# Performance work log

Measured on AMD Instinct MI355X. Metric: run time of the kernel, lower is better.

## Reference

```python
import jax, jax.numpy as jnp
import numpy as np


def _lstm_cell(x, h, c, w_ih, w_hh, b_ih, b_hh):
    # PyTorch LSTMCell gate order: i, f, g, o
    z = x @ w_ih.T + h @ w_hh.T + b_ih + b_hh
    i, f, g, o = jnp.split(z, 4, axis=-1)
    c_new = jax.nn.sigmoid(f) * c + jax.nn.sigmoid(i) * jnp.tanh(g)
    h_new = jax.nn.sigmoid(o) * jnp.tanh(c_new)
    return h_new, c_new


def setup_inputs() -> dict:
    B, T_in, T_out = 32, 512, 512
    n_mel, n_frames = 80, 1
    n_enc, n_att, n_filt, K = 512, 128, 32, 31
    n_arnn, n_drnn, n_pre = 1024, 1024, 256
    keys = jax.random.split(jax.random.key(0), 25)
    r = lambda k, *s: jax.random.normal(keys[k], s, dtype=jnp.float32) * 0.05
    return {
        "memory": jax.random.normal(keys[0], (B, T_in, n_enc), dtype=jnp.float32),
        "decoder_inputs": jax.random.normal(keys[1], (B, n_mel, T_out), dtype=jnp.float32),
        "memory_lengths": jax.random.randint(keys[2], (B,), T_in // 2, T_in + 1).astype(jnp.int32),
        "prenet_w1": r(3, n_pre, n_mel * n_frames),
        "prenet_w2": r(4, n_pre, n_pre),
        "arnn_w_ih": r(5, 4 * n_arnn, n_pre + n_enc),
        "arnn_w_hh": r(6, 4 * n_arnn, n_arnn),
        "arnn_b_ih": r(7, 4 * n_arnn),
        "arnn_b_hh": r(8, 4 * n_arnn),
        "query_w": r(9, n_att, n_arnn),
        "memory_w": r(10, n_att, n_enc),
        "v_w": r(11, 1, n_att),
        "loc_conv_w": r(12, n_filt, 2, K),
        "loc_dense_w": r(13, n_att, n_filt),
        "drnn_w_ih": r(14, 4 * n_drnn, n_arnn + n_enc),
        "drnn_w_hh": r(15, 4 * n_drnn, n_drnn),
        "drnn_b_ih": r(16, 4 * n_drnn),
        "drnn_b_hh": r(17, 4 * n_drnn),
        "proj_w": r(18, n_mel * n_frames, n_drnn + n_enc),
        "proj_b": r(19, n_mel * n_frames),
        "gate_w": r(20, 1, n_drnn + n_enc),
        "gate_b": r(21, 1),
    }


def reference(memory, decoder_inputs, memory_lengths, prenet_w1, prenet_w2,
              arnn_w_ih, arnn_w_hh, arnn_b_ih, arnn_b_hh,
              query_w, memory_w, v_w, loc_conv_w, loc_dense_w,
              drnn_w_ih, drnn_w_hh, drnn_b_ih, drnn_b_hh,
              proj_w, proj_b, gate_w, gate_b):
    B, T_in, n_enc = memory.shape
    n_mel, T_out = decoder_inputs.shape[1], decoder_inputs.shape[2]
    n_arnn = arnn_w_hh.shape[1]
    n_drnn = drnn_w_hh.shape[1]
    K = loc_conv_w.shape[-1]
    dt = memory.dtype

    # mask: True = padded position (masked_fill with -inf in torch)
    mask = jnp.arange(T_in)[None, :] >= memory_lengths[:, None]          # (B, T_in)
    processed_memory = memory @ memory_w.T                               # (B, T_in, n_att)

    # teacher-forced inputs with go frame: (T_out+1, B, n_mel)
    go = jnp.zeros((1, B, n_mel), dt)
    dec_in = jnp.concatenate([go, jnp.transpose(decoder_inputs, (2, 0, 1))], 0)
    # prenet (dropout omitted for a deterministic reference)
    pre = jax.nn.relu(dec_in @ prenet_w1.T)
    pre = jax.nn.relu(pre @ prenet_w2.T)[:-1]                            # (T_out, B, n_pre)

    init = (jnp.zeros((B, n_arnn), dt), jnp.zeros((B, n_arnn), dt),
            jnp.zeros((B, n_drnn), dt), jnp.zeros((B, n_drnn), dt),
            jnp.zeros((B, T_in), dt), jnp.zeros((B, T_in), dt),
            jnp.zeros((B, n_enc), dt))

    def step(carry, pre_t):
        ah, ac, dh, dc, aw, aw_cum, actx = carry
        # attention RNN
        ah, ac = _lstm_cell(jnp.concatenate([pre_t, actx], -1), ah, ac,
                            arnn_w_ih, arnn_w_hh, arnn_b_ih, arnn_b_hh)
        # location-sensitive attention
        aw_cat = jnp.stack([aw, aw_cum], axis=1)                         # (B, 2, T_in)
        loc = jax.lax.conv_general_dilated(
            aw_cat, loc_conv_w, (1,), [(K // 2, K // 2)],
            dimension_numbers=("NCH", "OIH", "NCH"))                   # (B, n_filt, T_in)
        loc = jnp.transpose(loc, (0, 2, 1)) @ loc_dense_w.T              # (B, T_in, n_att)
        pq = (ah @ query_w.T)[:, None, :]                                # (B, 1, n_att)
        e = (jnp.tanh(pq + loc + processed_memory) @ v_w.T)[..., 0]      # (B, T_in)
        e = jnp.where(mask, -jnp.inf, e)
        aw = jax.nn.softmax(e, axis=1)
        actx = jnp.einsum("bt,bte->be", aw, memory)                      # (B, n_enc)
        aw_cum = aw_cum + aw
        # decoder RNN
        dh, dc = _lstm_cell(jnp.concatenate([ah, actx], -1), dh, dc,
                            drnn_w_ih, drnn_w_hh, drnn_b_ih, drnn_b_hh)
        dhc = jnp.concatenate([dh, actx], -1)
        mel = dhc @ proj_w.T + proj_b
        gate = (dhc @ gate_w.T + gate_b)[:, 0]
        return (ah, ac, dh, dc, aw, aw_cum, actx), (mel, gate, aw)

    _, (mels, gates, aligns) = jax.lax.scan(step, init, pre)
    mel_outputs = jnp.transpose(mels, (1, 2, 0))        # (B, n_mel, T_out)
    gate_outputs = gates.T                              # (B, T_out)
    alignments = jnp.transpose(aligns, (1, 0, 2))       # (B, T_out, T_in)
    return mel_outputs, gate_outputs, alignments
```

## Files before the change

kernel.cpp:

```cpp
#include <hip/hip_runtime.h>
#include <math.h>

#define NB 32
#define TIN 512
#define TOUT 512
#define NENC 512
#define NATT 128
#define NU 1024
#define NG 4096
#define NPRE 256
#define NMEL 80

#define WS_AH    0u
#define WS_AC    32768u
#define WS_DH    65536u
#define WS_DC    98304u
#define WS_ACTX  131072u
#define WS_AW    147456u
#define WS_AWCUM 163840u
#define WS_E     180224u
#define WS_PQ    196608u
#define WS_ZD    200704u
#define WS_ZA    2822144u
#define WS_PM    4657152u
#define WS_PRE   6754304u
#define WS_WBF   10956800u
#define WS_STATE_ZERO_BYTES (200704u * 4u)
#define OUT_ALIGN ((size_t)NB * NMEL * TOUT + (size_t)NB * TOUT)

#define BW_DIH 0u
#define BW_DHH 6291456u
#define BW_AIH 10485760u
#define BW_AHH 13631488u

__device__ __forceinline__ float fsigm(float x) { return 1.f / (1.f + __expf(-x)); }
__device__ __forceinline__ float ftanh(float x) { return 1.f - 2.f / (__expf(2.f * x) + 1.f); }
__device__ __forceinline__ float bf2f(unsigned short h) { return __uint_as_float((unsigned)h << 16); }

__global__ __launch_bounds__(256) void packbf_kernel(const float* __restrict__ src,
                                                     unsigned short* __restrict__ dst, int n) {
    for (int i = blockIdx.x * 256 + threadIdx.x; i < n; i += gridDim.x * 256) {
        unsigned u = __float_as_uint(src[i]);
        dst[i] = (unsigned short)((u + 0x7FFFu + ((u >> 16) & 1u)) >> 16);
    }
}

__global__ __launch_bounds__(256) void prenet1_kernel(const float* __restrict__ dec,
                                                      const float* __restrict__ w1,
                                                      float* __restrict__ pre) {
    int t = blockIdx.x;
    __shared__ float xl[NB][NMEL];
    for (int i = threadIdx.x; i < NB * NMEL; i += 256) {
        int b = i / NMEL, m = i % NMEL;
        xl[b][m] = (t == 0) ? 0.0f : dec[(b * NMEL + m) * TOUT + (t - 1)];
    }
    __syncthreads();
    int j = threadIdx.x;
    float acc[NB];
#pragma unroll
    for (int b = 0; b < NB; b++) acc[b] = 0.0f;
    for (int m = 0; m < NMEL; m++) {
        float w = w1[j * NMEL + m];
#pragma unroll
        for (int b = 0; b < NB; b++) acc[b] += xl[b][m] * w;
    }
    for (int b = 0; b < NB; b++) pre[((size_t)t * NB + b) * NPRE + j] = fmaxf(acc[b], 0.0f);
}

__global__ __launch_bounds__(256) void prenet2_kernel(const float* __restrict__ w2,
                                                      float* __restrict__ pre) {
    int t = blockIdx.x;
    __shared__ float hl[NB][NPRE];
    for (int i = threadIdx.x; i < NB * NPRE; i += 256)
        hl[i / NPRE][i % NPRE] = pre[(size_t)t * NB * NPRE + i];
    __syncthreads();
    int j = threadIdx.x;
    float acc[NB];
#pragma unroll
    for (int b = 0; b < NB; b++) acc[b] = 0.0f;
    for (int k = 0; k < NPRE; k++) {
        float w = w2[j * NPRE + k];
#pragma unroll
        for (int b = 0; b < NB; b++) acc[b] += hl[b][k] * w;
    }
    for (int b = 0; b < NB; b++) pre[((size_t)t * NB + b) * NPRE + j] = fmaxf(acc[b], 0.0f);
}

__global__ __launch_bounds__(128) void pm_kernel(const float* __restrict__ mem,
                                                 const float* __restrict__ mw,
                                                 float* __restrict__ pm) {
    int b = blockIdx.y, t0 = blockIdx.x * 4;
    __shared__ float ml[4][NENC];
    for (int i = threadIdx.x; i < 4 * NENC; i += 128)
        ml[i / NENC][i % NENC] = mem[((size_t)b * TIN + t0 + i / NENC) * NENC + (i % NENC)];
    __syncthreads();
    int a = threadIdx.x;
    float acc[4] = {0, 0, 0, 0};
    for (int e = 0; e < NENC; e++) {
        float w = mw[a * NENC + e];
#pragma unroll
        for (int tt = 0; tt < 4; tt++) acc[tt] += ml[tt][e] * w;
    }
    for (int tt = 0; tt < 4; tt++)
        pm[((size_t)b * TIN + t0 + tt) * NATT + a] = acc[tt];
}

__global__ __launch_bounds__(256) void z_fused_kernel(
        const unsigned short* __restrict__ wbf,
        const float* __restrict__ ws_base, const float* __restrict__ pre_t,
        float* __restrict__ zd, float* __restrict__ za, int sbase) {
    int col = blockIdx.x * 256 + threadIdx.x;
    int s = blockIdx.y + sbase;
    const float* ah   = ws_base + WS_AH;
    const float* dh   = ws_base + WS_DH;
    const float* actx = ws_base + WS_ACTX;
    const unsigned short* W; const float* x; int xs;
    if (s < 8)       { W = wbf + BW_DIH + (size_t)col * 1536 + s * 128;              x = ah + s * 128;           xs = NU;   }
    else if (s < 12) { W = wbf + BW_DIH + (size_t)col * 1536 + 1024 + (s - 8) * 128; x = actx + (s - 8) * 128;   xs = NENC; }
    else if (s < 20) { W = wbf + BW_DHH + (size_t)col * 1024 + (s - 12) * 128;       x = dh + (s - 12) * 128;    xs = NU;   }
    else if (s < 22) { W = wbf + BW_AIH + (size_t)col * 768 + (s - 20) * 128;        x = pre_t + (s - 20) * 128; xs = NPRE; }
    else if (s < 26) { W = wbf + BW_AIH + (size_t)col * 768 + 256 + (s - 22) * 128;  x = actx + (s - 22) * 128;  xs = NENC; }
    else             { W = wbf + BW_AHH + (size_t)col * 1024 + (s - 26) * 128;       x = ah + (s - 26) * 128;    xs = NU;   }

    float acc[NB];
#pragma unroll
    for (int b = 0; b < NB; b++) acc[b] = 0.0f;
    for (int k4 = 0; k4 < 32; k4++) {
        ushort4 h4 = *(const ushort4*)(W + k4 * 4);
        float w0 = bf2f(h4.x), w1 = bf2f(h4.y), w2 = bf2f(h4.z), w3 = bf2f(h4.w);
#pragma unroll
        for (int b = 0; b < NB; b++) {
            float4 x4 = *(const float4*)(x + (size_t)b * xs + k4 * 4);
            acc[b] = fmaf(w0, x4.x, acc[b]);
            acc[b] = fmaf(w1, x4.y, acc[b]);
            acc[b] = fmaf(w2, x4.z, acc[b]);
            acc[b] = fmaf(w3, x4.w, acc[b]);
        }
    }
    float* zp = ((s < 20) ? (zd + (size_t)s * NB * NG) : (za + (size_t)(s - 20) * NB * NG)) + col;
#pragma unroll
    for (int b = 0; b < NB; b++) zp[(size_t)b * NG] = acc[b];
}

__global__ __launch_bounds__(128) void energies_kernel(const float* __restrict__ pm,
                                                       const float* __restrict__ wc,
                                                       const float* __restrict__ ldw,
                                                       const float* __restrict__ vw,
                                                       const int* __restrict__ mlen,
                                                       const float* __restrict__ ws_aw,
                                                       const float* __restrict__ ws_awcum,
                                                       const float* __restrict__ ws_pq,
                                                       float* __restrict__ ws_e) {
    int b = blockIdx.y, tc = blockIdx.x;
    int tt = threadIdx.x & 31, sub = threadIdx.x >> 5;
    int t = tc * 32 + tt;
    __shared__ float awl[TIN], cuml[TIN], locl[32][33], pql[NATT], ep[32][4];
    for (int i = threadIdx.x; i < TIN; i += 128) {
        awl[i]  = ws_aw[b * TIN + i];
        cuml[i] = ws_awcum[b * TIN + i];
    }
    for (int i = threadIdx.x; i < NATT; i += 128) pql[i] = ws_pq[b * NATT + i];
    __syncthreads();
    for (int f = sub * 8; f < sub * 8 + 8; f++) {
        float s = 0.0f;
        const float* wA = wc + f * 62;
        const float* wB = wA + 31;
        for (int d = 0; d < 31; d++) {
            int tp = t + d - 15;
            if (tp >= 0 && tp < TIN) s += awl[tp] * wA[d] + cuml[tp] * wB[d];
        }
        locl[tt][f] = s;
    }
    __syncthreads();
    float acc = 0.0f;
    const float* pmb = pm + ((size_t)b * TIN + t) * NATT;
    for (int a = sub * 32; a < sub * 32 + 32; a++) {
        float s = pql[a] + pmb[a];
        const float* lw = ldw + a * 32;
#pragma unroll
        for (int f = 0; f < 32; f++) s += locl[tt][f] * lw[f];
        acc += tanhf(s) * vw[a];
    }
    ep[tt][sub] = acc;
    __syncthreads();
    if (sub == 0) {
        float ev = ep[tt][0] + ep[tt][1] + ep[tt][2] + ep[tt][3];
        if (t >= mlen[b]) ev = -3.0e38f;
        ws_e[b * TIN + t] = ev;
    }
}

__global__ __launch_bounds__(256) void softmax_ctx_kernel(const float* __restrict__ mem,
                                                          const float* __restrict__ E,
                                                          float* __restrict__ AW,
                                                          float* __restrict__ AWCUM,
                                                          float* __restrict__ ACTX,
                                                          float* __restrict__ out_align, int step) {
    int b = blockIdx.y, ec = blockIdx.x;
    __shared__ float el[TIN];
    __shared__ float red[256];
    __shared__ float part[4][64];
    const float* Eb = E + b * TIN;
    for (int i = threadIdx.x; i < TIN; i += 256) el[i] = Eb[i];
    __syncthreads();
    red[threadIdx.x] = fmaxf(el[threadIdx.x], el[threadIdx.x + 256]);
    __syncthreads();
    for (int s = 128; s > 0; s >>= 1) {
        if (threadIdx.x < s) red[threadIdx.x] = fmaxf(red[threadIdx.x], red[threadIdx.x + s]);
        __syncthreads();
    }
    float mx = red[0];
    __syncthreads();
    float p0 = __expf(el[threadIdx.x] - mx), p1 = __expf(el[threadIdx.x + 256] - mx);
    el[threadIdx.x] = p0; el[threadIdx.x + 256] = p1;
    red[threadIdx.x] = p0 + p1;
    __syncthreads();
    for (int s = 128; s > 0; s >>= 1) {
        if (threadIdx.x < s) red[threadIdx.x] += red[threadIdx.x + s];
        __syncthreads();
    }
    float inv = 1.0f / red[0];
    int ei = ec * 64 + (threadIdx.x & 63), tp4 = threadIdx.x >> 6;
    float acc = 0.0f;
    const float* mb = mem + (size_t)b * TIN * NENC + ei;
    for (int t = tp4 * 128; t < tp4 * 128 + 128; t++) acc += el[t] * mb[(size_t)t * NENC];
    part[tp4][threadIdx.x & 63] = acc;
    __syncthreads();
    if (threadIdx.x < 64) {
        float ctx = (part[0][threadIdx.x] + part[1][threadIdx.x] +
                     part[2][threadIdx.x] + part[3][threadIdx.x]) * inv;
        ACTX[b * NENC + ec * 64 + threadIdx.x] = ctx;
    }
    if (ec == 0) {
        for (int i = threadIdx.x; i < TIN; i += 256) {
            float a_ = el[i] * inv;
            AW[b * TIN + i] = a_;
            AWCUM[b * TIN + i] += a_;
            out_align[((size_t)b * TOUT + step) * TIN + i] = a_;
        }
    }
}

__global__ __launch_bounds__(512) void gates_kernel(
        const float* __restrict__ abih, const float* __restrict__ abhh,
        const float* __restrict__ qw,
        const float* __restrict__ dbih, const float* __restrict__ dbhh,
        const float* __restrict__ pjw, const float* __restrict__ pjb,
        const float* __restrict__ gtw, const float* __restrict__ gtb,
        float* __restrict__ ws, float* __restrict__ out, int t) {
    __shared__ float sm[NU + NENC];
    int tid = threadIdx.x, bid = blockIdx.x;
    if (bid < 32) {
        if (t < 0) return;
        int b = bid;
        float* DH = ws + WS_DH + (size_t)b * NU;
        float* DC = ws + WS_DC + (size_t)b * NU;
        for (int u = tid; u < NU; u += 512) {
            float zi = dbih[u]          + dbhh[u];
            float zf = dbih[NU + u]     + dbhh[NU + u];
            float zg = dbih[2 * NU + u] + dbhh[2 * NU + u];
            float zo = dbih[3 * NU + u] + dbhh[3 * NU + u];
            for (int s = 0; s < 20; s++) {
                const float* z = ws + WS_ZD + ((size_t)s * NB + b) * NG;
                zi += z[u]; zf += z[NU + u]; zg += z[2 * NU + u]; zo += z[3 * NU + u];
            }
            float c = fsigm(zf) * DC[u] + fsigm(zi) * ftanh(zg);
            float h = fsigm(zo) * ftanh(c);
            DC[u] = c; DH[u] = h; sm[u] = h;
        }
        for (int i = tid; i < NENC; i += 512) sm[NU + i] = ws[WS_ACTX + b * NENC + i];
        __syncthreads();
        int col = tid >> 2, q = tid & 3;
        if (col < 81) {
            const float* wr = (col < 80) ? (pjw + (size_t)col * 1536) : gtw;
            const float* d4 = sm + q * 384;
            const float* w4 = wr + q * 384;
            float s = 0.f;
#pragma unroll
            for (int k4 = 0; k4 < 96; k4++) {
                float4 hv = *(const float4*)(d4 + k4 * 4);
                float4 wv = *(const float4*)(w4 + k4 * 4);
                s = fmaf(hv.x, wv.x, s); s = fmaf(hv.y, wv.y, s);
                s = fmaf(hv.z, wv.z, s); s = fmaf(hv.w, wv.w, s);
            }
            s += __shfl_xor(s, 1); s += __shfl_xor(s, 2);
            if (q == 0) {
                s += (col < 80) ? pjb[col] : gtb[0];
                if (col < 80) out[((size_t)b * NMEL + col) * TOUT + t] = s;
                else          out[(size_t)NB * NMEL * TOUT + (size_t)b * TOUT + t] = s;
            }
        }
    } else {
        int b = bid - 32;
        float* AH = ws + WS_AH + (size_t)b * NU;
        float* AC = ws + WS_AC + (size_t)b * NU;
        for (int u = tid; u < NU; u += 512) {
            float zi = abih[u]          + abhh[u];
            float zf = abih[NU + u]     + abhh[NU + u];
            float zg = abih[2 * NU + u] + abhh[2 * NU + u];
            float zo = abih[3 * NU + u] + abhh[3 * NU + u];
            for (int s = 0; s < 14; s++) {
                const float* z = ws + WS_ZA + ((size_t)s * NB + b) * NG;
                zi += z[u]; zf += z[NU + u]; zg += z[2 * NU + u]; zo += z[3 * NU + u];
            }
            float c = fsigm(zf) * AC[u] + fsigm(zi) * ftanh(zg);
            float h = fsigm(zo) * ftanh(c);
            AC[u] = c; AH[u] = h; sm[u] = h;
        }
        __syncthreads();
        int a = tid >> 2, q = tid & 3;
        if (a < NATT) {
            const float* qr = qw + (size_t)a * NU + q * 256;
            const float* h4 = sm + q * 256;
            float s = 0.f;
#pragma unroll
            for (int k4 = 0; k4 < 64; k4++) {
                float4 hv = *(const float4*)(h4 + k4 * 4);
                float4 wv = *(const float4*)(qr + k4 * 4);
                s = fmaf(hv.x, wv.x, s); s = fmaf(hv.y, wv.y, s);
                s = fmaf(hv.z, wv.z, s); s = fmaf(hv.w, wv.w, s);
            }
            s += __shfl_xor(s, 1); s += __shfl_xor(s, 2);
            if (q == 0) ws[WS_PQ + b * NATT + a] = s;
        }
    }
}

extern "C" void kernel_launch(void* const* d_in, const int* in_sizes, int n_in,
                              void* d_out, int out_size, void* d_ws, size_t ws_size,
                              hipStream_t stream) {
    const float* memory = (const float*)d_in[0];
    const float* dec    = (const float*)d_in[1];
    const int*   mlen   = (const int*)d_in[2];
    const float* pw1    = (const float*)d_in[3];
    const float* pw2    = (const float*)d_in[4];
    const float* awih   = (const float*)d_in[5];
    const float* awhh   = (const float*)d_in[6];
    const float* abih   = (const float*)d_in[7];
    const float* abhh   = (const float*)d_in[8];
    const float* qw     = (const float*)d_in[9];
    const float* mw     = (const float*)d_in[10];
    const float* vw     = (const float*)d_in[11];
    const float* wc     = (const float*)d_in[12];
    const float* ldw    = (const float*)d_in[13];
    const float* dwih   = (const float*)d_in[14];
    const float* dwhh   = (const float*)d_in[15];
    const float* dbih   = (const float*)d_in[16];
    const float* dbhh   = (const float*)d_in[17];
    const float* pjw    = (const float*)d_in[18];
    const float* pjb    = (const float*)d_in[19];
    const float* gtw    = (const float*)d_in[20];
    const float* gtb    = (const float*)d_in[21];
    float* ws  = (float*)d_ws;
    float* out = (float*)d_out;
    float* out_align = out + OUT_ALIGN;
    unsigned short* wbf = (unsigned short*)(ws + WS_WBF);

    hipMemsetAsync(ws, 0, WS_STATE_ZERO_BYTES, stream);
    hipMemsetAsync(ws + WS_PRE + (size_t)512 * NB * NPRE, 0, (size_t)NB * NPRE * 4, stream);

    packbf_kernel<<<1024, 256, 0, stream>>>(dwih, wbf + BW_DIH, 4096 * 1536);
    packbf_kernel<<<1024, 256, 0, stream>>>(dwhh, wbf + BW_DHH, 4096 * 1024);
    packbf_kernel<<<1024, 256, 0, stream>>>(awih, wbf + BW_AIH, 4096 * 768);
    packbf_kernel<<<1024, 256, 0, stream>>>(awhh, wbf + BW_AHH, 4096 * 1024);

    prenet1_kernel<<<TOUT, 256, 0, stream>>>(dec, pw1, ws + WS_PRE);
    prenet2_kernel<<<TOUT, 256, 0, stream>>>(pw2, ws + WS_PRE);
    pm_kernel<<<dim3(TIN / 4, NB), 128, 0, stream>>>(memory, mw, ws + WS_PM);

    z_fused_kernel<<<dim3(16, 14), 256, 0, stream>>>(
        wbf, ws, ws + WS_PRE, ws + WS_ZD, ws + WS_ZA, 20);
    gates_kernel<<<64, 512, 0, stream>>>(abih, abhh, qw, dbih, dbhh, pjw, pjb,
                                         gtw, gtb, ws, out, -1);

    for (int t = 0; t < TOUT; ++t) {
        energies_kernel<<<dim3(16, NB), 128, 0, stream>>>(
            ws + WS_PM, wc, ldw, vw, mlen,
            ws + WS_AW, ws + WS_AWCUM, ws + WS_PQ, ws + WS_E);
        softmax_ctx_kernel<<<dim3(8, NB), 256, 0, stream>>>(
            memory, ws + WS_E, ws + WS_AW, ws + WS_AWCUM, ws + WS_ACTX, out_align, t);
        z_fused_kernel<<<dim3(16, 34), 256, 0, stream>>>(
            wbf, ws, ws + WS_PRE + (size_t)(t + 1) * NB * NPRE,
            ws + WS_ZD, ws + WS_ZA, 0);
        gates_kernel<<<64, 512, 0, stream>>>(abih, abhh, qw, dbih, dbhh, pjw, pjb,
                                             gtw, gtb, ws, out, t);
    }
}
```

Baseline: 95.71 ms.

## Merge per-step kernels into two launches with intra-kernel flag synchronization

After: 120.0 ms. 1.25x slower.

```diff
diff --git a/kernel.cpp b/kernel.cpp
--- a/kernel.cpp
+++ b/kernel.cpp
@@ -20,12 +20,13 @@
 #define WS_AWCUM 163840u
 #define WS_E     180224u
 #define WS_PQ    196608u
-#define WS_ZD    200704u
-#define WS_ZA    2822144u
-#define WS_PM    4657152u
-#define WS_PRE   6754304u
-#define WS_WBF   10956800u
-#define WS_STATE_ZERO_BYTES (200704u * 4u)
+#define WS_FLG   200704u
+#define WS_ZD    217088u
+#define WS_ZA    2838528u
+#define WS_PM    4673536u
+#define WS_PRE   6770688u
+#define WS_WBF   10973184u
+#define WS_STATE_ZERO_BYTES (WS_ZD * 4u)
 #define OUT_ALIGN ((size_t)NB * NMEL * TOUT + (size_t)NB * TOUT)
 
 #define BW_DIH 0u
@@ -36,6 +37,10 @@
 __device__ __forceinline__ float fsigm(float x) { return 1.f / (1.f + __expf(-x)); }
 __device__ __forceinline__ float ftanh(float x) { return 1.f - 2.f / (__expf(2.f * x) + 1.f); }
 __device__ __forceinline__ float bf2f(unsigned short h) { return __uint_as_float((unsigned)h << 16); }
+
+__device__ __forceinline__ void st_wt(float* p, float v) {
+    asm volatile("global_store_dword %0, %1, off sc0 sc1" :: "v"(p), "v"(v) : "memory");
+}
 
 __global__ __launch_bounds__(256) void packbf_kernel(const float* __restrict__ src,
                                                      unsigned short* __restrict__ dst, int n) {
@@ -105,12 +110,10 @@
         pm[((size_t)b * TIN + t0 + tt) * NATT + a] = acc[tt];
 }
 
-__global__ __launch_bounds__(256) void z_fused_kernel(
+__device__ __forceinline__ void z_slice_body(
         const unsigned short* __restrict__ wbf,
         const float* __restrict__ ws_base, const float* __restrict__ pre_t,
-        float* __restrict__ zd, float* __restrict__ za, int sbase) {
-    int col = blockIdx.x * 256 + threadIdx.x;
-    int s = blockIdx.y + sbase;
+        float* __restrict__ zd, float* __restrict__ za, int s, int col, int wt) {
     const float* ah   = ws_base + WS_AH;
     const float* dh   = ws_base + WS_DH;
     const float* actx = ws_base + WS_ACTX;
@@ -138,107 +141,263 @@
         }
     }
     float* zp = ((s < 20) ? (zd + (size_t)s * NB * NG) : (za + (size_t)(s - 20) * NB * NG)) + col;
-#pragma unroll
-    for (int b = 0; b < NB; b++) zp[(size_t)b * NG] = acc[b];
-}
-
-__global__ __launch_bounds__(128) void energies_kernel(const float* __restrict__ pm,
-                                                       const float* __restrict__ wc,
-                                                       const float* __restrict__ ldw,
-                                                       const float* __restrict__ vw,
-                                                       const int* __restrict__ mlen,
-                                                       const float* __restrict__ ws_aw,
-                                                       const float* __restrict__ ws_awcum,
-                                                       const float* __restrict__ ws_pq,
-                                                       float* __restrict__ ws_e) {
-    int b = blockIdx.y, tc = blockIdx.x;
-    int tt = threadIdx.x & 31, sub = threadIdx.x >> 5;
+    if (wt) {
+#pragma unroll
+        for (int b = 0; b < NB; b++) st_wt(&zp[(size_t)b * NG], acc[b]);
+    } else {
+#pragma unroll
+        for (int b = 0; b < NB; b++) zp[(size_t)b * NG] = acc[b];
+    }
+}
+
+__global__ __launch_bounds__(128) void la_kernel(
+        const unsigned short* __restrict__ wbf, const float* __restrict__ pre_t1,
+        const float* __restrict__ wc, const float* __restrict__ ldw,
+        const float* __restrict__ vw, const int* __restrict__ mlen,
+        float* __restrict__ ws) {
+    __shared__ float sm[2336];
+    int tid = threadIdx.x, bid = blockIdx.x;
+    if (bid < 832) {
+        int sidx = bid >> 5;
+        int s = sidx < 8 ? sidx : (sidx < 18 ? sidx + 4 : sidx + 8);
+        z_slice_body(wbf, ws, pre_t1, ws + WS_ZD, ws + WS_ZA, s, (bid & 31) * 128 + tid, 0);
+        return;
+    }
+    int eb = bid - 832;
+    int b = eb >> 4, tc = eb & 15;
+    int tt = tid & 31, sub = tid >> 5;
     int t = tc * 32 + tt;
-    __shared__ float awl[TIN], cuml[TIN], locl[32][33], pql[NATT], ep[32][4];
-    for (int i = threadIdx.x; i < TIN; i += 128) {
-        awl[i]  = ws_aw[b * TIN + i];
-        cuml[i] = ws_awcum[b * TIN + i];
-    }
-    for (int i = threadIdx.x; i < NATT; i += 128) pql[i] = ws_pq[b * NATT + i];
+    float* awl  = sm;
+    float* cuml = sm + 512;
+    float* locl = sm + 1024;
+    float* pql  = sm + 2080;
+    float* ep   = sm + 2208;
+    for (int i = tid; i < TIN; i += 128) {
+        awl[i]  = ws[WS_AW + b * TIN + i];
+        cuml[i] = ws[WS_AWCUM + b * TIN + i];
+    }
+    for (int i = tid; i < NATT; i += 128) pql[i] = ws[WS_PQ + b * NATT + i];
     __syncthreads();
     for (int f = sub * 8; f < sub * 8 + 8; f++) {
-        float s = 0.0f;
+        float s_ = 0.0f;
         const float* wA = wc + f * 62;
         const float* wB = wA + 31;
         for (int d = 0; d < 31; d++) {
             int tp = t + d - 15;
-            if (tp >= 0 && tp < TIN) s += awl[tp] * wA[d] + cuml[tp] * wB[d];
-        }
-        locl[tt][f] = s;
+            if (tp >= 0 && tp < TIN) s_ += awl[tp] * wA[d] + cuml[tp] * wB[d];
+        }
+        locl[tt * 33 + f] = s_;
     }
     __syncthreads();
     float acc = 0.0f;
-    const float* pmb = pm + ((size_t)b * TIN + t) * NATT;
+    const float* pmb = ws + WS_PM + ((size_t)b * TIN + t) * NATT;
     for (int a = sub * 32; a < sub * 32 + 32; a++) {
-        float s = pql[a] + pmb[a];
+        float s_ = pql[a] + pmb[a];
         const float* lw = ldw + a * 32;
 #pragma unroll
-        for (int f = 0; f < 32; f++) s += locl[tt][f] * lw[f];
-        acc += tanhf(s) * vw[a];
-    }
-    ep[tt][sub] = acc;
+        for (int f = 0; f < 32; f++) s_ += locl[tt * 33 + f] * lw[f];
+        acc += tanhf(s_) * vw[a];
+    }
+    ep[tt * 4 + sub] = acc;
     __syncthreads();
     if (sub == 0) {
-        float ev = ep[tt][0] + ep[tt][1] + ep[tt][2] + ep[tt][3];
+        float ev = ep[tt * 4] + ep[tt * 4 + 1] + ep[tt * 4 + 2] + ep[tt * 4 + 3];
         if (t >= mlen[b]) ev = -3.0e38f;
-        ws_e[b * TIN + t] = ev;
-    }
-}
-
-__global__ __launch_bounds__(256) void softmax_ctx_kernel(const float* __restrict__ mem,
-                                                          const float* __restrict__ E,
-                                                          float* __restrict__ AW,
-                                                          float* __restrict__ AWCUM,
-                                                          float* __restrict__ ACTX,
-                                                          float* __restrict__ out_align, int step) {
-    int b = blockIdx.y, ec = blockIdx.x;
-    __shared__ float el[TIN];
-    __shared__ float red[256];
-    __shared__ float part[4][64];
-    const float* Eb = E + b * TIN;
-    for (int i = threadIdx.x; i < TIN; i += 256) el[i] = Eb[i];
-    __syncthreads();
-    red[threadIdx.x] = fmaxf(el[threadIdx.x], el[threadIdx.x + 256]);
-    __syncthreads();
-    for (int s = 128; s > 0; s >>= 1) {
-        if (threadIdx.x < s) red[threadIdx.x] = fmaxf(red[threadIdx.x], red[threadIdx.x + s]);
-        __syncthreads();
-    }
-    float mx = red[0];
-    __syncthreads();
-    float p0 = __expf(el[threadIdx.x] - mx), p1 = __expf(el[threadIdx.x + 256] - mx);
-    el[threadIdx.x] = p0; el[threadIdx.x + 256] = p1;
-    red[threadIdx.x] = p0 + p1;
-    __syncthreads();
-    for (int s = 128; s > 0; s >>= 1) {
-        if (threadIdx.x < s) red[threadIdx.x] += red[threadIdx.x + s];
-        __syncthreads();
-    }
-    float inv = 1.0f / red[0];
-    int ei = ec * 64 + (threadIdx.x & 63), tp4 = threadIdx.x >> 6;
-    float acc = 0.0f;
-    const float* mb = mem + (size_t)b * TIN * NENC + ei;
-    for (int t = tp4 * 128; t < tp4 * 128 + 128; t++) acc += el[t] * mb[(size_t)t * NENC];
-    part[tp4][threadIdx.x & 63] = acc;
-    __syncthreads();
-    if (threadIdx.x < 64) {
-        float ctx = (part[0][threadIdx.x] + part[1][threadIdx.x] +
-                     part[2][threadIdx.x] + part[3][threadIdx.x]) * inv;
-        ACTX[b * NENC + ec * 64 + threadIdx.x] = ctx;
-    }
-    if (ec == 0) {
-        for (int i = threadIdx.x; i < TIN; i += 256) {
-            float a_ = el[i] * inv;
-            AW[b * TIN + i] = a_;
-            AWCUM[b * TIN + i] += a_;
-            out_align[((size_t)b * TOUT + step) * TIN + i] = a_;
-        }
-    }
+        ws[WS_E + b * TIN + t] = ev;
+    }
+}
+
+__device__ void gates_body(const float* __restrict__ abih, const float* __restrict__ abhh,
+                           const float* __restrict__ qw,
+                           const float* __restrict__ dbih, const float* __restrict__ dbhh,
+                           const float* __restrict__ pjw, const float* __restrict__ pjb,
+                           const float* __restrict__ gtw, const float* __restrict__ gtb,
+                           float* __restrict__ ws, float* __restrict__ out, int t,
+                           int poll, unsigned* zxf, int gid, int tid, float* sm) {
+    if (gid < 32) {
+        if (t < 0) return;
+        int b = gid;
+        float* DH = ws + WS_DH + (size_t)b * NU;
+        float* DC = ws + WS_DC + (size_t)b * NU;
+        float zi[2], zf[2], zg[2], zo[2];
+#pragma unroll
+        for (int j = 0; j < 2; ++j) {
+            int u = tid + j * 512;
+            zi[j] = dbih[u]          + dbhh[u];
+            zf[j] = dbih[NU + u]     + dbhh[NU + u];
+            zg[j] = dbih[2 * NU + u] + dbhh[2 * NU + u];
+            zo[j] = dbih[3 * NU + u] + dbhh[3 * NU + u];
+            for (int s = 0; s < 20; ++s) {
+                if (s >= 8 && s < 12) continue;
+                const float* z = ws + WS_ZD + ((size_t)s * NB + b) * NG;
+                zi[j] += z[u]; zf[j] += z[NU + u]; zg[j] += z[2 * NU + u]; zo[j] += z[3 * NU + u];
+            }
+        }
+        if (poll && tid == 0) {
+            while (__hip_atomic_fetch_add(zxf, 0u, __ATOMIC_RELAXED, __HIP_MEMORY_SCOPE_AGENT) < 64u)
+                __builtin_amdgcn_s_sleep(8);
+        }
+        __syncthreads();
+#pragma unroll
+        for (int j = 0; j < 2; ++j) {
+            int u = tid + j * 512;
+            for (int s = 8; s < 12; ++s) {
+                const float* z = ws + WS_ZD + ((size_t)s * NB + b) * NG;
+                zi[j] += z[u]; zf[j] += z[NU + u]; zg[j] += z[2 * NU + u]; zo[j] += z[3 * NU + u];
+            }
+            float c = fsigm(zf[j]) * DC[u] + fsigm(zi[j]) * ftanh(zg[j]);
+            float h = fsigm(zo[j]) * ftanh(c);
+            DC[u] = c; DH[u] = h; sm[u] = h;
+        }
+        sm[NU + tid] = ws[WS_ACTX + b * NENC + tid];
+        __syncthreads();
+        int col = tid >> 2, q = tid & 3;
+        if (col < 81) {
+            const float* wr = (col < 80) ? (pjw + (size_t)col * 1536) : gtw;
+            const float* d4 = sm + q * 384;
+            const float* w4 = wr + q * 384;
+            float s_ = 0.f;
+#pragma unroll
+            for (int k4 = 0; k4 < 96; k4++) {
+                float4 hv = *(const float4*)(d4 + k4 * 4);
+                float4 wv = *(const float4*)(w4 + k4 * 4);
+                s_ = fmaf(hv.x, wv.x, s_); s_ = fmaf(hv.y, wv.y, s_);
+                s_ = fmaf(hv.z, wv.z, s_); s_ = fmaf(hv.w, wv.w, s_);
+            }
+            s_ += __shfl_xor(s_, 1); s_ += __shfl_xor(s_, 2);
+            if (q == 0) {
+                s_ += (col < 80) ? pjb[col] : gtb[0];
+                if (col < 80) out[((size_t)b * NMEL + col) * TOUT + t] = s_;
+                else          out[(size_t)NB * NMEL * TOUT + (size_t)b * TOUT + t] = s_;
+            }
+        }
+    } else {
+        int b = gid - 32;
+        float* AH = ws + WS_AH + (size_t)b * NU;
+        float* AC = ws + WS_AC + (size_t)b * NU;
+        float zi[2], zf[2], zg[2], zo[2];
+#pragma unroll
+        for (int j = 0; j < 2; ++j) {
+            int u = tid + j * 512;
+            zi[j] = abih[u]          + abhh[u];
+            zf[j] = abih[NU + u]     + abhh[NU + u];
+            zg[j] = abih[2 * NU + u] + abhh[2 * NU + u];
+            zo[j] = abih[3 * NU + u] + abhh[3 * NU + u];
+            for (int sA = 0; sA < 14; ++sA) {
+                if (sA >= 2 && sA < 6) continue;
+                const float* z = ws + WS_ZA + ((size_t)sA * NB + b) * NG;
+                zi[j] += z[u]; zf[j] += z[NU + u]; zg[j] += z[2 * NU + u]; zo[j] += z[3 * NU + u];
+            }
+        }
+        if (poll && tid == 0) {
+            while (__hip_atomic_fetch_add(zxf, 0u, __ATOMIC_RELAXED, __HIP_MEMORY_SCOPE_AGENT) < 64u)
+                __builtin_amdgcn_s_sleep(8);
+        }
+        __syncthreads();
+#pragma unroll
+        for (int j = 0; j < 2; ++j) {
+            int u = tid + j * 512;
+            for (int sA = 2; sA < 6; ++sA) {
+                const float* z = ws + WS_ZA + ((size_t)sA * NB + b) * NG;
+                zi[j] += z[u]; zf[j] += z[NU + u]; zg[j] += z[2 * NU + u]; zo[j] += z[3 * NU + u];
+            }
+            float c = fsigm(zf[j]) * AC[u] + fsigm(zi[j]) * ftanh(zg[j]);
+            float h = fsigm(zo[j]) * ftanh(c);
+            AC[u] = c; AH[u] = h; sm[u] = h;
+        }
+        __syncthreads();
+        int a = tid >> 2, q = tid & 3;
+        if (a < NATT) {
+            const float* qr = qw + (size_t)a * NU + q * 256;
+            const float* h4 = sm + q * 256;
+            float s_ = 0.f;
+#pragma unroll
+            for (int k4 = 0; k4 < 64; k4++) {
+                float4 hv = *(const float4*)(h4 + k4 * 4);
+                float4 wv = *(const float4*)(qr + k4 * 4);
+                s_ = fmaf(hv.x, wv.x, s_); s_ = fmaf(hv.y, wv.y, s_);
+                s_ = fmaf(hv.z, wv.z, s_); s_ = fmaf(hv.w, wv.w, s_);
+            }
+            s_ += __shfl_xor(s_, 1); s_ += __shfl_xor(s_, 2);
+            if (q == 0) ws[WS_PQ + b * NATT + a] = s_;
+        }
+    }
+}
+
+__global__ __launch_bounds__(512) void lb_kernel(
+        const unsigned short* __restrict__ wbf, const float* __restrict__ memory,
+        const float* __restrict__ abih, const float* __restrict__ abhh,
+        const float* __restrict__ qw,
+        const float* __restrict__ dbih, const float* __restrict__ dbhh,
+        const float* __restrict__ pjw, const float* __restrict__ pjb,
+        const float* __restrict__ gtw, const float* __restrict__ gtb,
+        float* __restrict__ ws, float* __restrict__ out, int t) {
+    __shared__ float sm[1552];
+    int tid = threadIdx.x, bid = blockIdx.x;
+    unsigned* smf = (unsigned*)(ws + WS_FLG) + t * 32;
+    unsigned* zxf = smf + 16;
+    if (bid < 128) {
+        int b = bid >> 2, ec = bid & 3;
+        float* el = sm; float* red = sm + 512; float* part = sm + 528;
+        float e0 = ws[WS_E + b * 512 + tid];
+        float m = e0;
+#pragma unroll
+        for (int sh = 1; sh <= 32; sh <<= 1) m = fmaxf(m, __shfl_xor(m, sh));
+        if ((tid & 63) == 0) red[tid >> 6] = m;
+        __syncthreads();
+        m = fmaxf(fmaxf(fmaxf(red[0], red[1]), fmaxf(red[2], red[3])),
+                  fmaxf(fmaxf(red[4], red[5]), fmaxf(red[6], red[7])));
+        float pv = __expf(e0 - m);
+        float ss = pv;
+#pragma unroll
+        for (int sh = 1; sh <= 32; sh <<= 1) ss += __shfl_xor(ss, sh);
+        if ((tid & 63) == 0) red[8 + (tid >> 6)] = ss;
+        __syncthreads();
+        float tot = red[8] + red[9] + red[10] + red[11] + red[12] + red[13] + red[14] + red[15];
+        float aw = pv / tot;
+        el[tid] = aw;
+        if (ec == 0) {
+            ws[WS_AW + b * 512 + tid] = aw;
+            ws[WS_AWCUM + b * 512 + tid] += aw;
+            (out + OUT_ALIGN)[((size_t)b * TOUT + t) * TIN + tid] = aw;
+        }
+        __syncthreads();
+        int e = tid & 127, tq = tid >> 7;
+        const float* mb = memory + (size_t)b * TIN * NENC + ec * 128 + e;
+        float acc = 0.f;
+        for (int u = tq * 128; u < tq * 128 + 128; ++u)
+            acc = fmaf(el[u], mb[(size_t)u * NENC], acc);
+        part[tq * 128 + e] = acc;
+        __syncthreads();
+        if (tid < 128)
+            st_wt(&ws[WS_ACTX + b * NENC + ec * 128 + tid],
+                  part[tid] + part[128 + tid] + part[256 + tid] + part[384 + tid]);
+        __syncthreads();
+        if (tid == 0)
+            __hip_atomic_fetch_add(smf, 1u, __ATOMIC_RELAXED, __HIP_MEMORY_SCOPE_AGENT);
+    } else if (bid < 192) {
+        int zi = bid - 128;
+        int sidx = zi >> 3;
+        int s = (sidx < 4) ? 8 + sidx : 18 + sidx;
+        if (tid == 0) {
+            while (__hip_atomic_fetch_add(smf, 0u, __ATOMIC_RELAXED, __HIP_MEMORY_SCOPE_AGENT) < 128u)
+                __builtin_amdgcn_s_sleep(8);
+        }
+        __syncthreads();
+        z_slice_body(wbf, ws, ws + WS_PRE, ws + WS_ZD, ws + WS_ZA, s, (zi & 7) * 512 + tid, 1);
+        __syncthreads();
+        if (tid == 0)
+            __hip_atomic_fetch_add(zxf, 1u, __ATOMIC_RELAXED, __HIP_MEMORY_SCOPE_AGENT);
+    } else {
+        gates_body(abih, abhh, qw, dbih, dbhh, pjw, pjb, gtw, gtb,
+                   ws, out, t, 1, zxf, bid - 192, tid, sm);
+    }
+}
+
+__global__ __launch_bounds__(128) void proz_kernel(const unsigned short* __restrict__ wbf,
+                                                   float* __restrict__ ws) {
+    z_slice_body(wbf, ws, ws + WS_PRE, ws + WS_ZD, ws + WS_ZA,
+                 20 + (int)blockIdx.y, (int)blockIdx.x * 128 + (int)threadIdx.x, 0);
 }
 
 __global__ __launch_bounds__(512) void gates_kernel(
@@ -248,82 +407,9 @@
         const float* __restrict__ pjw, const float* __restrict__ pjb,
         const float* __restrict__ gtw, const float* __restrict__ gtb,
         float* __restrict__ ws, float* __restrict__ out, int t) {
-    __shared__ float sm[NU + NENC];
-    int tid = threadIdx.x, bid = blockIdx.x;
-    if (bid < 32) {
-        if (t < 0) return;
-        int b = bid;
-        float* DH = ws + WS_DH + (size_t)b * NU;
-        float* DC = ws + WS_DC + (size_t)b * NU;
-        for (int u = tid; u < NU; u += 512) {
-            float zi = dbih[u]          + dbhh[u];
-            float zf = dbih[NU + u]     + dbhh[NU + u];
-            float zg = dbih[2 * NU + u] + dbhh[2 * NU + u];
-            float zo = dbih[3 * NU + u] + dbhh[3 * NU + u];
-            for (int s = 0; s < 20; s++) {
-                const float* z = ws + WS_ZD + ((size_t)s * NB + b) * NG;
-                zi += z[u]; zf += z[NU + u]; zg += z[2 * NU + u]; zo += z[3 * NU + u];
-            }
-            float c = fsigm(zf) * DC[u] + fsigm(zi) * ftanh(zg);
-            float h = fsigm(zo) * ftanh(c);
-            DC[u] = c; DH[u] = h; sm[u] = h;
-        }
-        for (int i = tid; i < NENC; i += 512) sm[NU + i] = ws[WS_ACTX + b * NENC + i];
-        __syncthreads();
-        int col = tid >> 2, q = tid & 3;
-        if (col < 81) {
-            const float* wr = (col < 80) ? (pjw + (size_t)col * 1536) : gtw;
-            const float* d4 = sm + q * 384;
-            const float* w4 = wr + q * 384;
-            float s = 0.f;
-#pragma unroll
-            for (int k4 = 0; k4 < 96; k4++) {
-                float4 hv = *(const float4*)(d4 + k4 * 4);
-                float4 wv = *(const float4*)(w4 + k4 * 4);
-                s = fmaf(hv.x, wv.x, s); s = fmaf(hv.y, wv.y, s);
-                s = fmaf(hv.z, wv.z, s); s = fmaf(hv.w, wv.w, s);
-            }
-            s += __shfl_xor(s, 1); s += __shfl_xor(s, 2);
-            if (q == 0) {
-                s += (col < 80) ? pjb[col] : gtb[0];
-                if (col < 80) out[((size_t)b * NMEL + col) * TOUT + t] = s;
-                else          out[(size_t)NB * NMEL * TOUT + (size_t)b * TOUT + t] = s;
-            }
-        }
-    } else {
-        int b = bid - 32;
-        float* AH = ws + WS_AH + (size_t)b * NU;
-        float* AC = ws + WS_AC + (size_t)b * NU;
-        for (int u = tid; u < NU; u += 512) {
-            float zi = abih[u]          + abhh[u];
-            float zf = abih[NU + u]     + abhh[NU + u];
-            float zg = abih[2 * NU + u] + abhh[2 * NU + u];
-            float zo = abih[3 * NU + u] + abhh[3 * NU + u];
-            for (int s = 0; s < 14; s++) {
-                const float* z = ws + WS_ZA + ((size_t)s * NB + b) * NG;
-                zi += z[u]; zf += z[NU + u]; zg += z[2 * NU + u]; zo += z[3 * NU + u];
-            }
-            float c = fsigm(zf) * AC[u] + fsigm(zi) * ftanh(zg);
-            float h = fsigm(zo) * ftanh(c);
-            AC[u] = c; AH[u] = h; sm[u] = h;
-        }
-        __syncthreads();
-        int a = tid >> 2, q = tid & 3;
-        if (a < NATT) {
-            const float* qr = qw + (size_t)a * NU + q * 256;
-            const float* h4 = sm + q * 256;
-            float s = 0.f;
-#pragma unroll
-            for (int k4 = 0; k4 < 64; k4++) {
-                float4 hv = *(const float4*)(h4 + k4 * 4);
-                float4 wv = *(const float4*)(qr + k4 * 4);
-                s = fmaf(hv.x, wv.x, s); s = fmaf(hv.y, wv.y, s);
-                s = fmaf(hv.z, wv.z, s); s = fmaf(hv.w, wv.w, s);
-            }
-            s += __shfl_xor(s, 1); s += __shfl_xor(s, 2);
-            if (q == 0) ws[WS_PQ + b * NATT + a] = s;
-        }
-    }
+    __shared__ float sm[1552];
+    gates_body(abih, abhh, qw, dbih, dbhh, pjw, pjb, gtw, gtb,
+               ws, out, t, 0, nullptr, (int)blockIdx.x, (int)threadIdx.x, sm);
 }
 
 extern "C" void kernel_launch(void* const* d_in, const int* in_sizes, int n_in,
@@ -353,7 +439,6 @@
     const float* gtb    = (const float*)d_in[21];
     float* ws  = (float*)d_ws;
     float* out = (float*)d_out;
-    float* out_align = out + OUT_ALIGN;
     unsigned short* wbf = (unsigned short*)(ws + WS_WBF);
 
     hipMemsetAsync(ws, 0, WS_STATE_ZERO_BYTES, stream);
@@ -368,21 +453,14 @@
     prenet2_kernel<<<TOUT, 256, 0, stream>>>(pw2, ws + WS_PRE);
     pm_kernel<<<dim3(TIN / 4, NB), 128, 0, stream>>>(memory, mw, ws + WS_PM);
 
-    z_fused_kernel<<<dim3(16, 14), 256, 0, stream>>>(
-        wbf, ws, ws + WS_PRE, ws + WS_ZD, ws + WS_ZA, 20);
+    proz_kernel<<<dim3(32, 14), 128, 0, stream>>>(wbf, ws);
     gates_kernel<<<64, 512, 0, stream>>>(abih, abhh, qw, dbih, dbhh, pjw, pjb,
                                          gtw, gtb, ws, out, -1);
 
     for (int t = 0; t < TOUT; ++t) {
-        energies_kernel<<<dim3(16, NB), 128, 0, stream>>>(
-            ws + WS_PM, wc, ldw, vw, mlen,
-            ws + WS_AW, ws + WS_AWCUM, ws + WS_PQ, ws + WS_E);
-        softmax_ctx_kernel<<<dim3(8, NB), 256, 0, stream>>>(
-            memory, ws + WS_E, ws + WS_AW, ws + WS_AWCUM, ws + WS_ACTX, out_align, t);
-        z_fused_kernel<<<dim3(16, 34), 256, 0, stream>>>(
-            wbf, ws, ws + WS_PRE + (size_t)(t + 1) * NB * NPRE,
-            ws + WS_ZD, ws + WS_ZA, 0);
-        gates_kernel<<<64, 512, 0, stream>>>(abih, abhh, qw, dbih, dbhh, pjw, pjb,
-                                             gtw, gtb, ws, out, t);
-    }
-}
+        la_kernel<<<1344, 128, 0, stream>>>(
+            wbf, ws + WS_PRE + (size_t)(t + 1) * NB * NPRE, wc, ldw, vw, mlen, ws);
+        lb_kernel<<<256, 512, 0, stream>>>(
+            wbf, memory, abih, abhh, qw, dbih, dbhh, pjw, pjb, gtw, gtb, ws, out, t);
+    }
+}
```

## Fuse attention energies into gates kernel with flag-based inter-block handoff

Applied to the files above, without the earlier changes.

Result: faster. 85.30 ms (-10.9%).

```diff
diff --git a/kernel.cpp b/kernel.cpp
--- a/kernel.cpp
+++ b/kernel.cpp
@@ -20,12 +20,13 @@
 #define WS_AWCUM 163840u
 #define WS_E     180224u
 #define WS_PQ    196608u
-#define WS_ZD    200704u
-#define WS_ZA    2822144u
-#define WS_PM    4657152u
-#define WS_PRE   6754304u
-#define WS_WBF   10956800u
-#define WS_STATE_ZERO_BYTES (200704u * 4u)
+#define WS_FLG   200704u
+#define WS_ZD    201728u
+#define WS_ZA    2823168u
+#define WS_PM    4658176u
+#define WS_PRE   6755328u
+#define WS_WBF   10957824u
+#define WS_STATE_ZERO_BYTES (WS_ZD * 4u)
 #define OUT_ALIGN ((size_t)NB * NMEL * TOUT + (size_t)NB * TOUT)
 
 #define BW_DIH 0u
@@ -36,6 +37,10 @@
 __device__ __forceinline__ float fsigm(float x) { return 1.f / (1.f + __expf(-x)); }
 __device__ __forceinline__ float ftanh(float x) { return 1.f - 2.f / (__expf(2.f * x) + 1.f); }
 __device__ __forceinline__ float bf2f(unsigned short h) { return __uint_as_float((unsigned)h << 16); }
+
+__device__ __forceinline__ void st_wt(float* p, float v) {
+    asm volatile("global_store_dword %0, %1, off sc0 sc1" :: "v"(p), "v"(v) : "memory");
+}
 
 __global__ __launch_bounds__(256) void packbf_kernel(const float* __restrict__ src,
                                                      unsigned short* __restrict__ dst, int n) {
@@ -105,12 +110,12 @@
         pm[((size_t)b * TIN + t0 + tt) * NATT + a] = acc[tt];
 }
 
-__global__ __launch_bounds__(256) void z_fused_kernel(
+__global__ __launch_bounds__(256) void z_all_kernel(
         const unsigned short* __restrict__ wbf,
         const float* __restrict__ ws_base, const float* __restrict__ pre_t,
-        float* __restrict__ zd, float* __restrict__ za, int sbase) {
+        float* __restrict__ zd, float* __restrict__ za) {
     int col = blockIdx.x * 256 + threadIdx.x;
-    int s = blockIdx.y + sbase;
+    int s = blockIdx.y;
     const float* ah   = ws_base + WS_AH;
     const float* dh   = ws_base + WS_DH;
     const float* actx = ws_base + WS_ACTX;
@@ -140,54 +145,6 @@
     float* zp = ((s < 20) ? (zd + (size_t)s * NB * NG) : (za + (size_t)(s - 20) * NB * NG)) + col;
 #pragma unroll
     for (int b = 0; b < NB; b++) zp[(size_t)b * NG] = acc[b];
-}
-
-__global__ __launch_bounds__(128) void energies_kernel(const float* __restrict__ pm,
-                                                       const float* __restrict__ wc,
-                                                       const float* __restrict__ ldw,
-                                                       const float* __restrict__ vw,
-                                                       const int* __restrict__ mlen,
-                                                       const float* __restrict__ ws_aw,
-                                                       const float* __restrict__ ws_awcum,
-                                                       const float* __restrict__ ws_pq,
-                                                       float* __restrict__ ws_e) {
-    int b = blockIdx.y, tc = blockIdx.x;
-    int tt = threadIdx.x & 31, sub = threadIdx.x >> 5;
-    int t = tc * 32 + tt;
-    __shared__ float awl[TIN], cuml[TIN], locl[32][33], pql[NATT], ep[32][4];
-    for (int i = threadIdx.x; i < TIN; i += 128) {
-        awl[i]  = ws_aw[b * TIN + i];
-        cuml[i] = ws_awcum[b * TIN + i];
-    }
-    for (int i = threadIdx.x; i < NATT; i += 128) pql[i] = ws_pq[b * NATT + i];
-    __syncthreads();
-    for (int f = sub * 8; f < sub * 8 + 8; f++) {
-        float s = 0.0f;
-        const float* wA = wc + f * 62;
-        const float* wB = wA + 31;
-        for (int d = 0; d < 31; d++) {
-            int tp = t + d - 15;
-            if (tp >= 0 && tp < TIN) s += awl[tp] * wA[d] + cuml[tp] * wB[d];
-        }
-        locl[tt][f] = s;
-    }
-    __syncthreads();
-    float acc = 0.0f;
-    const float* pmb = pm + ((size_t)b * TIN + t) * NATT;
-    for (int a = sub * 32; a < sub * 32 + 32; a++) {
-        float s = pql[a] + pmb[a];
-        const float* lw = ldw + a * 32;
-#pragma unroll
-        for (int f = 0; f < 32; f++) s += locl[tt][f] * lw[f];
-        acc += tanhf(s) * vw[a];
-    }
-    ep[tt][sub] = acc;
-    __syncthreads();
-    if (sub == 0) {
-        float ev = ep[tt][0] + ep[tt][1] + ep[tt][2] + ep[tt][3];
-        if (t >= mlen[b]) ev = -3.0e38f;
-        ws_e[b * TIN + t] = ev;
-    }
 }
 
 __global__ __launch_bounds__(256) void softmax_ctx_kernel(const float* __restrict__ mem,
@@ -241,15 +198,19 @@
     }
 }
 
-__global__ __launch_bounds__(512) void gates_kernel(
+__global__ __launch_bounds__(512) void ge_kernel(
         const float* __restrict__ abih, const float* __restrict__ abhh,
         const float* __restrict__ qw,
         const float* __restrict__ dbih, const float* __restrict__ dbhh,
         const float* __restrict__ pjw, const float* __restrict__ pjb,
         const float* __restrict__ gtw, const float* __restrict__ gtb,
+        const float* __restrict__ wc, const float* __restrict__ ldw,
+        const float* __restrict__ vw, const int* __restrict__ mlen,
         float* __restrict__ ws, float* __restrict__ out, int t) {
-    __shared__ float sm[NU + NENC];
+    __shared__ float sm[5888];
     int tid = threadIdx.x, bid = blockIdx.x;
+    unsigned* flg = (unsigned*)(ws + WS_FLG) + (t + 1);
+
     if (bid < 32) {
         if (t < 0) return;
         int b = bid;
@@ -290,7 +251,10 @@
                 else          out[(size_t)NB * NMEL * TOUT + (size_t)b * TOUT + t] = s;
             }
         }
-    } else {
+        return;
+    }
+    if (bid < 64) {
+        if (t + 1 >= TOUT) return;
         int b = bid - 32;
         float* AH = ws + WS_AH + (size_t)b * NU;
         float* AC = ws + WS_AC + (size_t)b * NU;
@@ -309,20 +273,82 @@
         }
         __syncthreads();
         int a = tid >> 2, q = tid & 3;
-        if (a < NATT) {
-            const float* qr = qw + (size_t)a * NU + q * 256;
-            const float* h4 = sm + q * 256;
-            float s = 0.f;
-#pragma unroll
-            for (int k4 = 0; k4 < 64; k4++) {
-                float4 hv = *(const float4*)(h4 + k4 * 4);
-                float4 wv = *(const float4*)(qr + k4 * 4);
-                s = fmaf(hv.x, wv.x, s); s = fmaf(hv.y, wv.y, s);
-                s = fmaf(hv.z, wv.z, s); s = fmaf(hv.w, wv.w, s);
-            }
-            s += __shfl_xor(s, 1); s += __shfl_xor(s, 2);
-            if (q == 0) ws[WS_PQ + b * NATT + a] = s;
-        }
+        const float* qr = qw + (size_t)a * NU + q * 256;
+        const float* h4 = sm + q * 256;
+        float s = 0.f;
+#pragma unroll
+        for (int k4 = 0; k4 < 64; k4++) {
+            float4 hv = *(const float4*)(h4 + k4 * 4);
+            float4 wv = *(const float4*)(qr + k4 * 4);
+            s = fmaf(hv.x, wv.x, s); s = fmaf(hv.y, wv.y, s);
+            s = fmaf(hv.z, wv.z, s); s = fmaf(hv.w, wv.w, s);
+        }
+        s += __shfl_xor(s, 1); s += __shfl_xor(s, 2);
+        if (q == 0) st_wt(&ws[WS_PQ + b * NATT + a], s);
+        __syncthreads();
+        if (tid == 0)
+            __hip_atomic_fetch_add(flg, 1u, __ATOMIC_RELAXED, __HIP_MEMORY_SCOPE_AGENT);
+        return;
+    }
+    if (t + 1 >= TOUT) return;
+    int eb = bid - 64;
+    int b = eb >> 2, tc = eb & 3;
+    int tt = tid & 127, sub = tid >> 7;
+    int tp_ = tc * 128 + tt;
+    float* awl  = sm;
+    float* cuml = sm + 512;
+    float* locl = sm + 1024;
+    float* pql  = sm + 5248;
+    float* ep   = sm + 5376;
+    for (int i = tid; i < TIN; i += 512) {
+        awl[i]  = ws[WS_AW + b * TIN + i];
+        cuml[i] = ws[WS_AWCUM + b * TIN + i];
+    }
+    if (tid == 0) {
+        while (__hip_atomic_fetch_add(flg, 0u, __ATOMIC_RELAXED, __HIP_MEMORY_SCOPE_AGENT) < 32u)
+            __builtin_amdgcn_s_sleep(8);
+    }
+    __syncthreads();
+    if (tid < NATT)
+        pql[tid] = __hip_atomic_load(&ws[WS_PQ + b * NATT + tid],
+                                     __ATOMIC_RELAXED, __HIP_MEMORY_SCOPE_AGENT);
+    __syncthreads();
+    {
+        int f0 = sub * 8;
+        float sA[8];
+#pragma unroll
+        for (int j = 0; j < 8; ++j) sA[j] = 0.f;
+        for (int d = 0; d < 31; ++d) {
+            int tp = tp_ + d - 15;
+            int tc_ = min(max(tp, 0), 511);
+            bool ok = (tp >= 0) && (tp < 512);
+            float a_ = ok ? awl[tc_] : 0.f;
+            float c_ = ok ? cuml[tc_] : 0.f;
+#pragma unroll
+            for (int j = 0; j < 8; ++j)
+                sA[j] = fmaf(a_, wc[(f0 + j) * 62 + d], fmaf(c_, wc[(f0 + j) * 62 + 31 + d], sA[j]));
+        }
+#pragma unroll
+        for (int j = 0; j < 8; ++j) locl[tt * 33 + f0 + j] = sA[j];
+    }
+    __syncthreads();
+    {
+        float acc = 0.0f;
+        const float* pmb = ws + WS_PM + ((size_t)b * TIN + tp_) * NATT;
+        for (int a = sub * 32; a < sub * 32 + 32; a++) {
+            float s_ = pql[a] + pmb[a];
+            const float* lw = ldw + a * 32;
+#pragma unroll
+            for (int f = 0; f < 32; f++) s_ += locl[tt * 33 + f] * lw[f];
+            acc += tanhf(s_) * vw[a];
+        }
+        ep[tt * 4 + sub] = acc;
+    }
+    __syncthreads();
+    if (sub == 0) {
+        float ev = ep[tt * 4] + ep[tt * 4 + 1] + ep[tt * 4 + 2] + ep[tt * 4 + 3];
+        if (tp_ >= mlen[b]) ev = -3.0e38f;
+        ws[WS_E + b * TIN + tp_] = ev;
     }
 }
 
@@ -368,21 +394,17 @@
     prenet2_kernel<<<TOUT, 256, 0, stream>>>(pw2, ws + WS_PRE);
     pm_kernel<<<dim3(TIN / 4, NB), 128, 0, stream>>>(memory, mw, ws + WS_PM);
 
-    z_fused_kernel<<<dim3(16, 14), 256, 0, stream>>>(
-        wbf, ws, ws + WS_PRE, ws + WS_ZD, ws + WS_ZA, 20);
-    gates_kernel<<<64, 512, 0, stream>>>(abih, abhh, qw, dbih, dbhh, pjw, pjb,
-                                         gtw, gtb, ws, out, -1);
+    z_all_kernel<<<dim3(16, 34), 256, 0, stream>>>(
+        wbf, ws, ws + WS_PRE, ws + WS_ZD, ws + WS_ZA);
+    ge_kernel<<<192, 512, 0, stream>>>(abih, abhh, qw, dbih, dbhh, pjw, pjb,
+                                       gtw, gtb, wc, ldw, vw, mlen, ws, out, -1);
 
     for (int t = 0; t < TOUT; ++t) {
-        energies_kernel<<<dim3(16, NB), 128, 0, stream>>>(
-            ws + WS_PM, wc, ldw, vw, mlen,
-            ws + WS_AW, ws + WS_AWCUM, ws + WS_PQ, ws + WS_E);
         softmax_ctx_kernel<<<dim3(8, NB), 256, 0, stream>>>(
             memory, ws + WS_E, ws + WS_AW, ws + WS_AWCUM, ws + WS_ACTX, out_align, t);
-        z_fused_kernel<<<dim3(16, 34), 256, 0, stream>>>(
-            wbf, ws, ws + WS_PRE + (size_t)(t + 1) * NB * NPRE,
-            ws + WS_ZD, ws + WS_ZA, 0);
-        gates_kernel<<<64, 512, 0, stream>>>(abih, abhh, qw, dbih, dbhh, pjw, pjb,
-                                             gtw, gtb, ws, out, t);
-    }
-}
+        z_all_kernel<<<dim3(16, 34), 256, 0, stream>>>(
+            wbf, ws, ws + WS_PRE + (size_t)(t + 1) * NB * NPRE, ws + WS_ZD, ws + WS_ZA);
+        ge_kernel<<<192, 512, 0, stream>>>(abih, abhh, qw, dbih, dbhh, pjw, pjb,
+                                           gtw, gtb, wc, ldw, vw, mlen, ws, out, t);
+    }
+}
```
